# Performance work log

Measured on AMD Instinct MI355X. Metric: run time of the kernel, lower is better.

## Reference

```python
import jax, jax.numpy as jnp
import numpy as np

NUM_HEADS = 8
CHANNELS = 512


def setup_inputs() -> dict:
    key = jax.random.key(0)
    k1, k2, k3, k4, k5 = jax.random.split(key, 5)
    C = CHANNELS
    x = jax.random.normal(k1, (8, C, 64, 64), dtype=jnp.float32)
    # 1x1 conv weights stored as (out_ch, in_ch) matrices
    qkv_w = jax.random.normal(k2, (3 * C, C), dtype=jnp.float32) * (C ** -0.5)
    qkv_b = jax.random.normal(k3, (3 * C,), dtype=jnp.float32) * 0.02
    proj_w = jax.random.normal(k4, (C, C), dtype=jnp.float32) * (C ** -0.5)
    proj_b = jax.random.normal(k5, (C,), dtype=jnp.float32) * 0.02
    return {"x": x, "qkv_w": qkv_w, "qkv_b": qkv_b, "proj_w": proj_w, "proj_b": proj_b}


def reference(x, qkv_w, qkv_b, proj_w, proj_b):
    B, C, H, W = x.shape
    heads = NUM_HEADS
    d = C // heads
    N = H * W
    scale = d ** -0.5
    # 1x1 conv == per-pixel matmul over channels
    qkv = jnp.einsum('bchw,oc->bohw', x, qkv_w) + qkv_b[None, :, None, None]
    qkv = qkv.reshape(B, 3, heads, d, N)
    q, k, v = qkv[:, 0], qkv[:, 1], qkv[:, 2]  # each (B, heads, d, N)
    # NOTE: attention over the channel dim -> (B, heads, d, d), as in the torch code
    attn = jax.nn.softmax(jnp.einsum('bhdn,bhen->bhde', q, k) * scale, axis=-1)
    # dropout is identity in eval mode
    out = jnp.einsum('bhde,bhen->bhdn', attn, v).reshape(B, C, H, W)
    out = jnp.einsum('bchw,oc->bohw', out, proj_w) + proj_b[None, :, None, None]
    return out, attn.mean(axis=1)  # (B,C,H,W), (B,d,d)
```

## Files before the change

kernel.cpp:

```cpp
#include <hip/hip_runtime.h>
#include <cstdio>
#include <cstdint>

#define BATCH 8
#define CH    512
#define OC3   1536
#define QKROWS 1024
#define NPIX  4096
#define HEADS 8
#define HDIM  64
#define KDEPTH 512
#define SCALE 0.125f
#define NSPLIT 16

typedef __bf16 bf16;
typedef __bf16 bf16x4 __attribute__((ext_vector_type(4)));
typedef __bf16 bf16x8 __attribute__((ext_vector_type(8)));
typedef float  f32x4  __attribute__((ext_vector_type(4)));

#define AS1 __attribute__((address_space(1)))
#define AS3 __attribute__((address_space(3)))

__global__ __launch_bounds__(256) void convert_bf16_kernel(
    const float* __restrict__ in, bf16* __restrict__ out, int n)
{
    const int i = blockIdx.x * 256 + threadIdx.x;
    if (i < n) out[i] = (bf16)in[i];
}

__global__ __launch_bounds__(256) void wvt_kernel(
    const bf16* __restrict__ wv, bf16* __restrict__ wvt)
{
    const int c0 = blockIdx.x * 64;
    const int d0 = blockIdx.y * 64;
    __shared__ bf16 tl[64][72];
    const int t = threadIdx.x;

    #pragma unroll
    for (int i = 0; i < 2; ++i) {
        const int lin = t + 256 * i;
        const int row = lin >> 3;
        const int c8  = (lin & 7) * 8;
        *(bf16x8*)&tl[row][c8] = *(const bf16x8*)(wv + (size_t)(d0 + row) * CH + c0 + c8);
    }
    __syncthreads();
    #pragma unroll
    for (int i = 0; i < 2; ++i) {
        const int lin  = t + 256 * i;
        const int crow = lin >> 3;
        const int d8   = (lin & 7) * 8;
        bf16x8 v;
        #pragma unroll
        for (int j = 0; j < 8; ++j) v[j] = tl[d8 + j][crow];
        *(bf16x8*)(wvt + (size_t)(c0 + crow) * CH + d0 + d8) = v;
    }
}

__global__ __launch_bounds__(256) void transpose_convert_kernel(
    const float* __restrict__ src, bf16* __restrict__ dst)
{
    const int b  = blockIdx.z;
    const int n0 = blockIdx.x * 64;
    const int c0 = blockIdx.y * 64;
    __shared__ float tile[64][65];
    const int t = threadIdx.x;
    const float* xp = src + (size_t)b * CH * NPIX;

    #pragma unroll
    for (int i = 0; i < 4; ++i) {
        const int lin = t + 256 * i;
        const int r   = lin >> 4;
        const int c4  = (lin & 15) * 4;
        const float4 v = *(const float4*)(xp + (size_t)(c0 + r) * 4096 + n0 + c4);
        tile[r][c4 + 0] = v.x; tile[r][c4 + 1] = v.y;
        tile[r][c4 + 2] = v.z; tile[r][c4 + 3] = v.w;
    }
    __syncthreads();

    bf16* op = dst + (size_t)b * NPIX * CH;
    #pragma unroll
    for (int i = 0; i < 2; ++i) {
        const int lin = t + 256 * i;
        const int n   = lin >> 3;
        const int c8  = (lin & 7) * 8;
        bf16x8 v;
        #pragma unroll
        for (int jj = 0; jj < 8; ++jj) v[jj] = (bf16)tile[c8 + jj][n];
        *(bf16x8*)(op + (size_t)(n0 + n) * CH + c0 + c8) = v;
    }
}

__global__ __launch_bounds__(256) void gemm_qk_kernel(
    const bf16* __restrict__ A, const bf16* __restrict__ Bt,
    const float* __restrict__ bias, bf16* __restrict__ qkb)
{
    const int b  = blockIdx.z;
    const int m0 = blockIdx.y * 128;
    const int n0 = blockIdx.x * 128;
    const bf16* Ap = A;
    const bf16* Bp = Bt + (size_t)b * NPIX * KDEPTH;

    __shared__ bf16 smem[16384];

    const int t    = threadIdx.x;
    const int lane = t & 63;
    const int wave = t >> 6;
    const int wr   = wave >> 1, wc = wave & 1;

    f32x4 acc[4][4];
    const f32x4 zf = {0.f, 0.f, 0.f, 0.f};
    #pragma unroll
    for (int i = 0; i < 4; ++i)
        #pragma unroll
        for (int j = 0; j < 4; ++j) acc[i][j] = zf;

    auto STAGE = [&](int p, int k0) {
        #pragma unroll
        for (int i = 0; i < 2; ++i) {
            const int c   = t + 256 * i;
            const int row = c >> 2;
            const int kb  = ((c & 3) ^ ((row >> 1) & 3)) * 8;
            __builtin_amdgcn_global_load_lds(
                (const AS1 void*)(Ap + (size_t)(m0 + row) * KDEPTH + k0 + kb),
                (AS3 void*)(smem + p * 8192 + c * 8), 16, 0, 0);
            __builtin_amdgcn_global_load_lds(
                (const AS1 void*)(Bp + (size_t)(n0 + row) * KDEPTH + k0 + kb),
                (AS3 void*)(smem + p * 8192 + 4096 + c * 8), 16, 0, 0);
        }
    };

    STAGE(0, 0);
    __syncthreads();
    int cur = 0;

    for (int kt = 0; kt < KDEPTH / 32; ++kt) {
        if (kt < KDEPTH / 32 - 1) STAGE(cur ^ 1, (kt + 1) * 32);

        const bf16* AsP = smem + cur * 8192;
        const bf16* BsP = AsP + 4096;
        bf16x8 af[4], bfv[4];
        #pragma unroll
        for (int i = 0; i < 4; ++i) {
            const int ar = wr * 64 + i * 16 + (lane & 15);
            const int ja = (lane >> 4) ^ ((ar >> 1) & 3);
            af[i]  = *(const bf16x8*)(AsP + ar * 32 + ja * 8);
            const int br = wc * 64 + i * 16 + (lane & 15);
            const int jb = (lane >> 4) ^ ((br >> 1) & 3);
            bfv[i] = *(const bf16x8*)(BsP + br * 32 + jb * 8);
        }
        #pragma unroll
        for (int i = 0; i < 4; ++i)
            #pragma unroll
            for (int j = 0; j < 4; ++j)
                acc[i][j] = __builtin_amdgcn_mfma_f32_16x16x32_bf16(
                    af[i], bfv[j], acc[i][j], 0, 0, 0);

        __syncthreads();
        cur ^= 1;
    }

    bf16* Qp = qkb + (size_t)b * QKROWS * NPIX;
    #pragma unroll
    for (int i = 0; i < 4; ++i) {
        const int mb = m0 + wr * 64 + i * 16 + (lane >> 4) * 4;
        #pragma unroll
        for (int r = 0; r < 4; ++r) {
            const int m  = mb + r;
            const float bv = bias[m];
            #pragma unroll
            for (int j = 0; j < 4; ++j) {
                const int n = n0 + wc * 64 + j * 16 + (lane & 15);
                Qp[(size_t)m * NPIX + n] = (bf16)(acc[i][j][r] + bv);
            }
        }
    }
}

__global__ __launch_bounds__(256) void qk_partial_kernel(
    const bf16* __restrict__ qk, float* __restrict__ part)
{
    const int s  = blockIdx.x;
    const int bh = blockIdx.y;
    const int b = bh >> 3, h = bh & 7;
    const bf16* qbase = qk + ((size_t)b * QKROWS + h * HDIM) * NPIX;
    const bf16* kbase = qk + ((size_t)b * QKROWS + CH + h * HDIM) * NPIX;

    __shared__ bf16 smem[16384];

    const int t    = threadIdx.x;
    const int lane = t & 63;
    const int wave = t >> 6;

    f32x4 acc[4];
    const f32x4 zf = {0.f, 0.f, 0.f, 0.f};
    #pragma unroll
    for (int j = 0; j < 4; ++j) acc[j] = zf;

    auto STAGE = [&](int p, int n0) {
        #pragma unroll
        for (int i = 0; i < 2; ++i) {
            const int c   = t + 256 * i;
            const int row = c >> 3;
            const int nb  = ((c & 7) ^ (row & 7)) * 8;
            __builtin_amdgcn_global_load_lds(
                (const AS1 void*)(qbase + (size_t)row * NPIX + n0 + nb),
                (AS3 void*)(smem + p * 8192 + c * 8), 16, 0, 0);
            __builtin_amdgcn_global_load_lds(
                (const AS1 void*)(kbase + (size_t)row * NPIX + n0 + nb),
                (AS3 void*)(smem + p * 8192 + 4096 + c * 8), 16, 0, 0);
        }
    };

    STAGE(0, s * 256);
    __syncthreads();
    int cur = 0;

    for (int nc = 0; nc < 4; ++nc) {
        if (nc < 3) STAGE(cur ^ 1, s * 256 + (nc + 1) * 64);

        const bf16* Qs = smem + cur * 8192;
        const bf16* Ks = Qs + 4096;
        #pragma unroll
        for (int ks = 0; ks < 2; ++ks) {
            const int dr = wave * 16 + (lane & 15);
            const int ja = (ks * 4 + (lane >> 4)) ^ (dr & 7);
            const bf16x8 af = *(const bf16x8*)(Qs + dr * 64 + ja * 8);
            #pragma unroll
            for (int j = 0; j < 4; ++j) {
                const int er = j * 16 + (lane & 15);
                const int jb = (ks * 4 + (lane >> 4)) ^ (er & 7);
                const bf16x8 bf_ = *(const bf16x8*)(Ks + er * 64 + jb * 8);
                acc[j] = __builtin_amdgcn_mfma_f32_16x16x32_bf16(af, bf_, acc[j], 0, 0, 0);
            }
        }
        __syncthreads();
        cur ^= 1;
    }

    float* pb = part + (((size_t)bh * NSPLIT + s) * 64) * 64;
    #pragma unroll
    for (int j = 0; j < 4; ++j)
        #pragma unroll
        for (int r = 0; r < 4; ++r)
            pb[(size_t)(wave * 16 + (lane >> 4) * 4 + r) * 64 + j * 16 + (lane & 15)] = acc[j][r];
}

__global__ __launch_bounds__(256) void qk_reduce_softmax_kernel(
    const float* __restrict__ part, float* __restrict__ attn)
{
    const int bh = blockIdx.x;
    const int t  = threadIdx.x;
    const int r  = t >> 2;
    const int e0 = (t & 3) * 16;

    float v[16];
    #pragma unroll
    for (int i = 0; i < 16; ++i) v[i] = 0.f;

    const float* pb = part + ((size_t)bh * NSPLIT * 64) * 64 + r * 64 + e0;
    for (int s = 0; s < NSPLIT; ++s) {
        const float* ps = pb + (size_t)s * 4096;
        #pragma unroll
        for (int c4 = 0; c4 < 4; ++c4) {
            const float4 p = *(const float4*)(ps + c4 * 4);
            v[c4 * 4 + 0] += p.x; v[c4 * 4 + 1] += p.y;
            v[c4 * 4 + 2] += p.z; v[c4 * 4 + 3] += p.w;
        }
    }

    float m = -1e30f;
    #pragma unroll
    for (int i = 0; i < 16; ++i) m = fmaxf(m, v[i]);
    m = fmaxf(m, __shfl_xor(m, 1));
    m = fmaxf(m, __shfl_xor(m, 2));

    float sum = 0.f;
    #pragma unroll
    for (int i = 0; i < 16; ++i) {
        v[i] = __expf((v[i] - m) * SCALE);
        sum += v[i];
    }
    sum += __shfl_xor(sum, 1);
    sum += __shfl_xor(sum, 2);
    const float inv = 1.f / sum;

    float* arow = attn + ((size_t)bh * 64 + r) * 64 + e0;
    #pragma unroll
    for (int c4 = 0; c4 < 4; ++c4) {
        float4 o;
        o.x = v[c4 * 4 + 0] * inv; o.y = v[c4 * 4 + 1] * inv;
        o.z = v[c4 * 4 + 2] * inv; o.w = v[c4 * 4 + 3] * inv;
        *(float4*)(arow + c4 * 4) = o;
    }
}

__global__ __launch_bounds__(256) void attn_mean_kernel(
    const float* __restrict__ attn, float* __restrict__ om)
{
    const int idx = blockIdx.x * 256 + threadIdx.x;
    const int b = idx >> 12, de = idx & 4095;
    float s = 0.f;
    #pragma unroll
    for (int h = 0; h < 8; ++h)
        s += attn[(((size_t)b * 8 + h) << 12) + de];
    om[idx] = s * 0.125f;
}

__global__ __launch_bounds__(256) void wprime_kernel(
    const float* __restrict__ proj_w, const float* __restrict__ attn,
    bf16* __restrict__ wp)
{
    const int o0 = blockIdx.x * 64;
    const int h  = blockIdx.y;
    const int b  = blockIdx.z;

    __shared__ float ws[64][65];
    __shared__ float as_[64][65];

    const int t = threadIdx.x;
    #pragma unroll
    for (int i = 0; i < 4; ++i) {
        const int lin = t + 256 * i;
        const int r   = lin >> 4;
        const int c4  = (lin & 15) * 4;
        const float4 wv = *(const float4*)(proj_w + (size_t)(o0 + r) * CH + h * HDIM + c4);
        ws[r][c4 + 0] = wv.x; ws[r][c4 + 1] = wv.y;
        ws[r][c4 + 2] = wv.z; ws[r][c4 + 3] = wv.w;
        const float4 av = *(const float4*)(attn + (((size_t)(b * 8 + h) * 64) + r) * 64 + c4);
        as_[r][c4 + 0] = av.x; as_[r][c4 + 1] = av.y;
        as_[r][c4 + 2] = av.z; as_[r][c4 + 3] = av.w;
    }
    __syncthreads();

    const int tx = t & 15, ty = t >> 4;
    const int to = ty * 4, te = tx * 4;
    float acc[4][4] = {};
    for (int d = 0; d < 64; ++d) {
        float a[4], bb[4];
        #pragma unroll
        for (int i = 0; i < 4; ++i) a[i]  = ws[to + i][d];
        #pragma unroll
        for (int j = 0; j < 4; ++j) bb[j] = as_[d][te + j];
        #pragma unroll
        for (int i = 0; i < 4; ++i)
            #pragma unroll
            for (int j = 0; j < 4; ++j)
                acc[i][j] = fmaf(a[i], bb[j], acc[i][j]);
    }

    bf16* wb = wp + (size_t)b * CH * CH;
    #pragma unroll
    for (int i = 0; i < 4; ++i)
        #pragma unroll
        for (int j = 0; j < 4; ++j)
            wb[(size_t)(o0 + to + i) * CH + h * HDIM + te + j] = (bf16)acc[i][j];
}

__global__ __launch_bounds__(256) void bias2_kernel(
    const bf16* __restrict__ wp, const float* __restrict__ bv,
    const float* __restrict__ pb, float* __restrict__ bias2)
{
    const int idx = blockIdx.x * 256 + threadIdx.x;
    const int b = idx >> 9, o = idx & 511;
    const bf16* wr = wp + ((size_t)b * CH + o) * CH;
    float s = 0.f;
    for (int d = 0; d < 512; ++d) s += (float)wr[d] * bv[d];
    bias2[idx] = s + pb[o];
}

__global__ __launch_bounds__(256) void gemm128_kernel(
    const bf16* __restrict__ A, const bf16* __restrict__ Bt,
    const float* __restrict__ bias, size_t bias_bstride,
    float* __restrict__ Cf, bf16* __restrict__ Cb,
    int ncols, int c_rows, size_t a_bstride, size_t bt_bstride)
{
    const int b  = blockIdx.z;
    const int m0 = blockIdx.y * 128;
    const int n0 = blockIdx.x * 128;
    const bf16* Ap = A  + (size_t)b * a_bstride;
    const bf16* Bp = Bt + (size_t)b * bt_bstride;

    __shared__ bf16 smem[16384];

    const int t    = threadIdx.x;
    const int lane = t & 63;
    const int wave = t >> 6;
    const int wr   = wave >> 1, wc = wave & 1;

    f32x4 acc[4][4];
    const f32x4 zf = {0.f, 0.f, 0.f, 0.f};
    #pragma unroll
    for (int i = 0; i < 4; ++i)
        #pragma unroll
        for (int j = 0; j < 4; ++j) acc[i][j] = zf;

    auto STAGE = [&](int p, int k0) {
        #pragma unroll
        for (int i = 0; i < 2; ++i) {
            const int c   = t + 256 * i;
            const int row = c >> 2;
            const int kb  = ((c & 3) ^ ((row >> 1) & 3)) * 8;
            __builtin_amdgcn_global_load_lds(
                (const AS1 void*)(Ap + (size_t)(m0 + row) * KDEPTH + k0 + kb),
                (AS3 void*)(smem + p * 8192 + c * 8), 16, 0, 0);
            __builtin_amdgcn_global_load_lds(
                (const AS1 void*)(Bp + (size_t)(n0 + row) * KDEPTH + k0 + kb),
                (AS3 void*)(smem + p * 8192 + 4096 + c * 8), 16, 0, 0);
        }
    };

    STAGE(0, 0);
    __syncthreads();
    int cur = 0;

    for (int kt = 0; kt < KDEPTH / 32; ++kt) {
        if (kt < KDEPTH / 32 - 1) STAGE(cur ^ 1, (kt + 1) * 32);

        const bf16* AsP = smem + cur * 8192;
        const bf16* BsP = AsP + 4096;
        bf16x8 af[4], bfv[4];
        #pragma unroll
        for (int i = 0; i < 4; ++i) {
            const int ar = wr * 64 + i * 16 + (lane & 15);
            const int ja = (lane >> 4) ^ ((ar >> 1) & 3);
            af[i]  = *(const bf16x8*)(AsP + ar * 32 + ja * 8);
            const int br = wc * 64 + i * 16 + (lane & 15);
            const int jb = (lane >> 4) ^ ((br >> 1) & 3);
            bfv[i] = *(const bf16x8*)(BsP + br * 32 + jb * 8);
        }
        #pragma unroll
        for (int i = 0; i < 4; ++i)
            #pragma unroll
            for (int j = 0; j < 4; ++j)
                acc[i][j] = __builtin_amdgcn_mfma_f32_16x16x32_bf16(
                    af[i], bfv[j], acc[i][j], 0, 0, 0);

        __syncthreads();
        cur ^= 1;
    }

    #pragma unroll
    for (int i = 0; i < 4; ++i) {
        const int mb = m0 + wr * 64 + i * 16 + (lane >> 4) * 4;
        #pragma unroll
        for (int r = 0; r < 4; ++r) {
            const int m  = mb + r;
            const float bv = bias ? bias[b * bias_bstride + m] : 0.f;
            #pragma unroll
            for (int j = 0; j < 4; ++j) {
                const int n = n0 + wc * 64 + j * 16 + (lane & 15);
                if (Cb) Cb[(size_t)b * c_rows * ncols + (size_t)m * ncols + n] =
                            (bf16)(acc[i][j][r] + bv);
                else    Cf[(size_t)b * c_rows * ncols + (size_t)m * ncols + n] =
                            acc[i][j][r] + bv;
            }
        }
    }
}

extern "C" void kernel_launch(void* const* d_in, const int* in_sizes, int n_in,
                              void* d_out, int out_size, void* d_ws, size_t ws_size,
                              hipStream_t stream)
{
    (void)in_sizes; (void)n_in; (void)out_size;
    const float* x      = (const float*)d_in[0];
    const float* qkv_w  = (const float*)d_in[1];
    const float* qkv_b  = (const float*)d_in[2];
    const float* proj_w = (const float*)d_in[3];
    const float* proj_b = (const float*)d_in[4];

    float* out       = (float*)d_out;
    float* attn_mean = out + (size_t)BATCH * CH * NPIX;

    const size_t qk_bytes   = (size_t)BATCH * QKROWS * NPIX * 2;
    const size_t xt_bytes   = (size_t)BATCH * NPIX * CH * 2;
    const size_t wq_bytes   = (size_t)OC3 * KDEPTH * 2;
    const size_t attn_bytes = (size_t)BATCH * HEADS * HDIM * HDIM * 4;
    const size_t part_bytes = (size_t)BATCH * HEADS * NSPLIT * HDIM * HDIM * 4;
    const size_t wp_bytes   = (size_t)BATCH * CH * CH * 2;
    const size_t wpp_bytes  = (size_t)BATCH * CH * CH * 2;
    const size_t wvt_bytes  = (size_t)CH * CH * 2;
    const size_t b2_bytes   = (size_t)BATCH * CH * 4;
    const size_t need = qk_bytes + xt_bytes + wq_bytes + attn_bytes + part_bytes +
                        wp_bytes + wpp_bytes + wvt_bytes + b2_bytes;
    if (ws_size < need) {
        fprintf(stderr, "[kernel_launch] ws_size=%zu < need=%zu — abort\n", ws_size, need);
        fflush(stderr);
        return;
    }

    char* p = (char*)d_ws;
    bf16*  qk     = (bf16*)p;             p += qk_bytes;
    bf16*  xt     = (bf16*)p;             p += xt_bytes;
    bf16*  wq_b   = (bf16*)p;             p += wq_bytes;
    float* attn   = (float*)p;            p += attn_bytes;
    float* part   = (float*)p;            p += part_bytes;
    bf16*  wprime = (bf16*)p;             p += wp_bytes;
    bf16*  wpp    = (bf16*)p;             p += wpp_bytes;
    bf16*  wvt    = (bf16*)p;             p += wvt_bytes;
    float* bias2  = (float*)p;

    convert_bf16_kernel<<<dim3((OC3 * KDEPTH + 255) / 256), 256, 0, stream>>>(
        qkv_w, wq_b, OC3 * KDEPTH);
    wvt_kernel<<<dim3(8, 8), 256, 0, stream>>>(wq_b + (size_t)2 * CH * KDEPTH, wvt);

    transpose_convert_kernel<<<dim3(NPIX / 64, CH / 64, BATCH), 256, 0, stream>>>(x, xt);

    gemm_qk_kernel<<<dim3(NPIX / 128, QKROWS / 128, BATCH), 256, 0, stream>>>(
        wq_b, xt, qkv_b, qk);

    qk_partial_kernel<<<dim3(NSPLIT, BATCH * HEADS), 256, 0, stream>>>(qk, part);
    qk_reduce_softmax_kernel<<<dim3(BATCH * HEADS), 256, 0, stream>>>(part, attn);

    attn_mean_kernel<<<dim3(BATCH * HDIM * HDIM / 256), 256, 0, stream>>>(attn, attn_mean);

    wprime_kernel<<<dim3(CH / 64, HEADS, BATCH), 256, 0, stream>>>(proj_w, attn, wprime);

    gemm128_kernel<<<dim3(CH / 128, CH / 128, BATCH), 256, 0, stream>>>(
        wprime, wvt, nullptr, 0, nullptr, wpp, CH, CH, (size_t)CH * CH, 0);
    bias2_kernel<<<dim3(BATCH * CH / 256), 256, 0, stream>>>(
        wprime, qkv_b + 2 * CH, proj_b, bias2);

    gemm128_kernel<<<dim3(NPIX / 128, CH / 128, BATCH), 256, 0, stream>>>(
        wpp, xt, bias2, CH, out, nullptr, NPIX, CH, (size_t)CH * CH,
        (size_t)NPIX * KDEPTH);
}
```

Before: 167.9 us.

## Stage GEMM epilogues through LDS for vectorized stores, remap workgroups, halve QK splits

The QK projection GEMM and the fp32 output GEMM now write their accumulator tiles into shared memory first, then emit 16-byte coalesced global stores instead of scattered 2- or 4-byte stores. Both GEMMs also remap the block index so consecutive workgroups are spread across XCD-sized groups, aiming for better L2 locality. The QK partial reduction uses half as many splits, each looping over twice the pixels, which cuts partial-sum traffic but reduces parallelism. The extra LDS round trip and barriers add some epilogue latency.

```diff
diff --git a/kernel.cpp b/kernel.cpp
--- a/kernel.cpp
+++ b/kernel.cpp
@@ -11,7 +11,7 @@
 #define HDIM  64
 #define KDEPTH 512
 #define SCALE 0.125f
-#define NSPLIT 16
+#define NSPLIT 8
 
 typedef __bf16 bf16;
 typedef __bf16 bf16x4 __attribute__((ext_vector_type(4)));
@@ -94,9 +94,15 @@
     const bf16* __restrict__ A, const bf16* __restrict__ Bt,
     const float* __restrict__ bias, bf16* __restrict__ qkb)
 {
+    const int nwg  = gridDim.x * gridDim.y;
+    const int orig = blockIdx.x + gridDim.x * blockIdx.y;
+    const int wg   = (orig & 7) * (nwg >> 3) + (orig >> 3);
+    const int by   = wg % gridDim.y;
+    const int bx   = wg / gridDim.y;
+
     const int b  = blockIdx.z;
-    const int m0 = blockIdx.y * 128;
-    const int n0 = blockIdx.x * 128;
+    const int m0 = by * 128;
+    const int n0 = bx * 128;
     const bf16* Ap = A;
     const bf16* Bp = Bt + (size_t)b * NPIX * KDEPTH;
 
@@ -159,19 +165,30 @@
         cur ^= 1;
     }
 
-    bf16* Qp = qkb + (size_t)b * QKROWS * NPIX;
-    #pragma unroll
-    for (int i = 0; i < 4; ++i) {
-        const int mb = m0 + wr * 64 + i * 16 + (lane >> 4) * 4;
-        #pragma unroll
-        for (int r = 0; r < 4; ++r) {
-            const int m  = mb + r;
-            const float bv = bias[m];
-            #pragma unroll
-            for (int j = 0; j < 4; ++j) {
-                const int n = n0 + wc * 64 + j * 16 + (lane & 15);
-                Qp[(size_t)m * NPIX + n] = (bf16)(acc[i][j][r] + bv);
+    {
+        bf16* ct = smem;
+        #pragma unroll
+        for (int i = 0; i < 4; ++i) {
+            const int ml = wr * 64 + i * 16 + (lane >> 4) * 4;
+            #pragma unroll
+            for (int r = 0; r < 4; ++r) {
+                const float bv = bias[m0 + ml + r];
+                #pragma unroll
+                for (int j = 0; j < 4; ++j) {
+                    const int n = wc * 64 + j * 16 + (lane & 15);
+                    ct[(ml + r) * 128 + n] = (bf16)(acc[i][j][r] + bv);
+                }
             }
+        }
+        __syncthreads();
+        bf16* Qp = qkb + (size_t)b * QKROWS * NPIX;
+        #pragma unroll
+        for (int ii = 0; ii < 8; ++ii) {
+            const int c   = t + 256 * ii;
+            const int row = c >> 4;
+            const int seg = c & 15;
+            const int4 v = *(const int4*)(ct + row * 128 + seg * 8);
+            *(int4*)(Qp + (size_t)(m0 + row) * NPIX + n0 + seg * 8) = v;
         }
     }
 }
@@ -211,12 +228,12 @@
         }
     };
 
-    STAGE(0, s * 256);
+    STAGE(0, s * 512);
     __syncthreads();
     int cur = 0;
 
-    for (int nc = 0; nc < 4; ++nc) {
-        if (nc < 3) STAGE(cur ^ 1, s * 256 + (nc + 1) * 64);
+    for (int nc = 0; nc < 8; ++nc) {
+        if (nc < 7) STAGE(cur ^ 1, s * 512 + (nc + 1) * 64);
 
         const bf16* Qs = smem + cur * 8192;
         const bf16* Ks = Qs + 4096;
@@ -374,9 +391,15 @@
     float* __restrict__ Cf, bf16* __restrict__ Cb,
     int ncols, int c_rows, size_t a_bstride, size_t bt_bstride)
 {
+    const int nwg  = gridDim.x * gridDim.y;
+    const int orig = blockIdx.x + gridDim.x * blockIdx.y;
+    const int wg   = (orig & 7) * (nwg >> 3) + (orig >> 3);
+    const int by   = wg % gridDim.y;
+    const int bx   = wg / gridDim.y;
+
     const int b  = blockIdx.z;
-    const int m0 = blockIdx.y * 128;
-    const int n0 = blockIdx.x * 128;
+    const int m0 = by * 128;
+    const int n0 = bx * 128;
     const bf16* Ap = A  + (size_t)b * a_bstride;
     const bf16* Bp = Bt + (size_t)b * bt_bstride;
 
@@ -439,21 +462,52 @@
         cur ^= 1;
     }
 
-    #pragma unroll
-    for (int i = 0; i < 4; ++i) {
-        const int mb = m0 + wr * 64 + i * 16 + (lane >> 4) * 4;
-        #pragma unroll
-        for (int r = 0; r < 4; ++r) {
-            const int m  = mb + r;
-            const float bv = bias ? bias[b * bias_bstride + m] : 0.f;
-            #pragma unroll
-            for (int j = 0; j < 4; ++j) {
-                const int n = n0 + wc * 64 + j * 16 + (lane & 15);
-                if (Cb) Cb[(size_t)b * c_rows * ncols + (size_t)m * ncols + n] =
-                            (bf16)(acc[i][j][r] + bv);
-                else    Cf[(size_t)b * c_rows * ncols + (size_t)m * ncols + n] =
-                            acc[i][j][r] + bv;
+    if (Cb) {
+        #pragma unroll
+        for (int i = 0; i < 4; ++i) {
+            const int mb = m0 + wr * 64 + i * 16 + (lane >> 4) * 4;
+            #pragma unroll
+            for (int r = 0; r < 4; ++r) {
+                const int m  = mb + r;
+                const float bv = bias ? bias[b * bias_bstride + m] : 0.f;
+                #pragma unroll
+                for (int j = 0; j < 4; ++j) {
+                    const int n = n0 + wc * 64 + j * 16 + (lane & 15);
+                    Cb[(size_t)b * c_rows * ncols + (size_t)m * ncols + n] =
+                        (bf16)(acc[i][j][r] + bv);
+                }
             }
+        }
+    } else {
+        float* ct = (float*)smem;
+        float* Cp = Cf + (size_t)b * c_rows * ncols;
+        #pragma unroll
+        for (int p = 0; p < 2; ++p) {
+            if (wc == p) {
+                #pragma unroll
+                for (int i = 0; i < 4; ++i) {
+                    const int ml = wr * 64 + i * 16 + (lane >> 4) * 4;
+                    #pragma unroll
+                    for (int r = 0; r < 4; ++r) {
+                        const float bv = bias ? bias[b * bias_bstride + m0 + ml + r] : 0.f;
+                        #pragma unroll
+                        for (int j = 0; j < 4; ++j) {
+                            const int n = j * 16 + (lane & 15);
+                            ct[(ml + r) * 64 + n] = acc[i][j][r] + bv;
+                        }
+                    }
+                }
+            }
+            __syncthreads();
+            #pragma unroll
+            for (int ii = 0; ii < 8; ++ii) {
+                const int c   = t + 256 * ii;
+                const int row = c >> 4;
+                const int seg = c & 15;
+                const float4 v = *(const float4*)(ct + row * 64 + seg * 4);
+                *(float4*)(Cp + (size_t)(m0 + row) * ncols + n0 + p * 64 + seg * 4) = v;
+            }
+            __syncthreads();
         }
     }
 }
```

Result: faster. 162.4 us (-3.3%).
